# Kernel tuning notes

Measured on AMD Instinct MI355X. Metric: run time of the kernel, lower is better.

## Reference

```python
import jax, jax.numpy as jnp
import numpy as np

B, HW, FEAT = 64, 196, 2048
EMB, HID, ATT, VOCAB, T = 512, 1024, 512, 10000, 20
STEPS = T - 1  # pack_padded_sequence uses lengths - 1


def setup_inputs() -> dict:
    key = jax.random.key(0)
    ks = jax.random.split(key, 16)
    rn = lambda k, s, sc=0.02: jax.random.normal(k, s, jnp.float32) * sc
    return {
        "features": jax.random.normal(ks[0], (B, HW, FEAT), jnp.float32),
        "captions": jax.random.randint(ks[1], (B, T), 0, VOCAB),
        "lengths": jnp.full((B,), T, jnp.int32),  # uniform lengths -> constant batch per step
        "E": rn(ks[2], (VOCAB, EMB)),
        "W_feat": rn(ks[3], (EMB, FEAT)), "b_feat": jnp.zeros((EMB,), jnp.float32),
        "W1": rn(ks[4], (ATT, EMB)), "b1": jnp.zeros((ATT,), jnp.float32),
        "W2": rn(ks[5], (ATT, HID)), "b2": jnp.zeros((ATT,), jnp.float32),
        "V": rn(ks[6], (1, ATT)), "bV": jnp.zeros((1,), jnp.float32),
        "W_hi": rn(ks[7], (HID, EMB)), "b_hi": jnp.zeros((HID,), jnp.float32),
        "W_ci": rn(ks[8], (HID, EMB)), "b_ci": jnp.zeros((HID,), jnp.float32),
        "W_ih": rn(ks[9], (4 * HID, 2 * EMB)), "b_ih": jnp.zeros((4 * HID,), jnp.float32),
        "W_hh": rn(ks[10], (4 * HID, HID)), "b_hh": jnp.zeros((4 * HID,), jnp.float32),
        "W_out": rn(ks[11], (VOCAB, HID)), "b_out": jnp.zeros((VOCAB,), jnp.float32),
    }


def reference(features, captions, lengths, E, W_feat, b_feat, W1, b1, W2, b2,
              V, bV, W_hi, b_hi, W_ci, b_ci, W_ih, b_ih, W_hh, b_hh, W_out, b_out):
    # features -> embed space: [B, HW, EMB]
    f = jnp.einsum('bhc,ec->bhe', features, W_feat) + b_feat
    fmean = f.mean(axis=1)                      # [B, EMB]
    hx0 = fmean @ W_hi.T + b_hi                 # [B, HID]
    cx0 = fmean @ W_ci.T + b_ci                 # [B, HID]
    fa = jnp.einsum('bhe,ae->bha', f, W1) + b1  # W1(features), [B, HW, ATT]

    emb = E[captions]                           # [B, T, EMB]
    xs = jnp.swapaxes(emb[:, :STEPS], 0, 1)     # [STEPS, B, EMB] teacher-forced inputs

    def step(carry, x):
        hx, cx = carry
        # Bahdanau attention
        ha = hx @ W2.T + b2                             # [B, ATT]
        score = jnp.tanh(fa + ha[:, None, :])           # [B, HW, ATT]
        logits = jnp.einsum('bha,oa->bho', score, V) + bV   # [B, HW, 1]
        w = jax.nn.softmax(logits, axis=1)              # softmax over HW
        ctx = jnp.sum(w * f, axis=1)                    # [B, EMB]
        # LSTMCell (PyTorch gate order: i, f, g, o)
        inp = jnp.concatenate([x, ctx], axis=1)         # [B, 2*EMB]
        gates = inp @ W_ih.T + b_ih + hx @ W_hh.T + b_hh
        i_g, f_g, g_g, o_g = jnp.split(gates, 4, axis=1)
        cx_n = jax.nn.sigmoid(f_g) * cx + jax.nn.sigmoid(i_g) * jnp.tanh(g_g)
        hx_n = jax.nn.sigmoid(o_g) * jnp.tanh(cx_n)
        out = hx_n @ W_out.T + b_out                    # dropout = identity (eval)
        return (hx_n, cx_n), out

    _, outs = jax.lax.scan(step, (hx0, cx0), xs)        # [STEPS, B, VOCAB]
    # torch.cat(outputs) over constant per-step batch == flatten time-major
    return outs.reshape(STEPS * B, VOCAB)
```

## Files before the change

### kernel.cpp

```cpp
#include <hip/hip_runtime.h>
#include <hip/hip_bf16.h>
#include <math.h>

#define BB 64
#define HW 196
#define FEAT 2048
#define EMB 512
#define HID 1024
#define ATT 512
#define VOCAB 10000
#define TT 20
#define STEPS 19

using bfrag = __attribute__((ext_vector_type(8))) short;
using f32x4 = __attribute__((ext_vector_type(4))) float;

__device__ __forceinline__ float sigmoid_fast(float x) { return 1.0f / (1.0f + __expf(-x)); }
__device__ __forceinline__ float tanh_fast(float x) {
    float e = __expf(2.0f * x);
    return 1.0f - 2.0f / (e + 1.0f);
}
__device__ __forceinline__ ushort f2bf_rne(float f) {
    unsigned u = __float_as_uint(f);
    unsigned r = (u + 0x7FFFu + ((u >> 16) & 1u)) >> 16;
    return (ushort)r;
}
__device__ __forceinline__ float bf2f(ushort h) {
    return __uint_as_float(((unsigned)h) << 16);
}
__device__ __forceinline__ int sw_idx(int row, int g) { return row * 4 + (g ^ ((row >> 1) & 3)); }

__global__ __launch_bounds__(256) void k_split(const float* __restrict__ x,
                                               ushort* __restrict__ hi,
                                               ushort* __restrict__ lo, int n)
{
    int i4 = (blockIdx.x * 256 + threadIdx.x) * 4;
    if (i4 >= n) return;
    float4 v = *(const float4*)(x + i4);
    float av[4] = {v.x, v.y, v.z, v.w};
    #pragma unroll
    for (int j = 0; j < 4; ++j) {
        ushort h = f2bf_rne(av[j]);
        hi[i4 + j] = h;
        lo[i4 + j] = f2bf_rne(av[j] - bf2f(h));
    }
}

template<bool NFAST>
__global__ __launch_bounds__(256) void mfma_g(
    const float* __restrict__ A,
    const ushort* __restrict__ Bhi, const ushort* __restrict__ Blo,
    const float* __restrict__ bias, float* __restrict__ C,
    int N, int K, int Bld, int ldc, int NXB, int NMB)
{
    __shared__ __align__(16) ushort sAh[256 * 8];
    __shared__ __align__(16) ushort sAl[256 * 8];
    __shared__ __align__(16) ushort sBh[512 * 8];
    __shared__ __align__(16) ushort sBl[512 * 8];

    const int tid = threadIdx.x;

    const int nwg = NXB * NMB;
    const int q = nwg >> 3, r = nwg & 7;
    const int xcd = blockIdx.x & 7, sidx = blockIdx.x >> 3;
    const int wg = (xcd < r) ? (xcd * (q + 1) + sidx)
                             : (r * (q + 1) + (xcd - r) * q + sidx);
    int im, inb;
    if (NFAST) { inb = wg % NXB; im = wg / NXB; }
    else       { im = wg % NMB; inb = wg / NMB; }
    const int m0 = im * 64;
    const int n0 = inb * 128;

    const int lane = tid & 63;
    const int w = tid >> 6;
    const int mh = (w & 1) * 32;
    const int nh = (w >> 1) * 64;
    const int g = lane >> 4, l15 = lane & 15;

    f32x4 acc[2][4] = {};

    for (int k0 = 0; k0 < K; k0 += 32) {
        __syncthreads();
        {
            int r_ = tid >> 2, g_ = tid & 3;
            const float* ap = A + (size_t)(m0 + r_) * K + k0 + g_ * 8;
            float av[8];
            *(float4*)(av)     = *(const float4*)(ap);
            *(float4*)(av + 4) = *(const float4*)(ap + 4);
            bfrag vh, vl;
            #pragma unroll
            for (int j = 0; j < 8; ++j) {
                ushort h = f2bf_rne(av[j]);
                vh[j] = (short)h;
                vl[j] = (short)f2bf_rne(av[j] - bf2f(h));
            }
            int c = sw_idx(r_, g_) * 8;
            *(bfrag*)&sAh[c] = vh;
            *(bfrag*)&sAl[c] = vl;
        }
        #pragma unroll
        for (int i = 0; i < 4; ++i) {
            int c = tid + i * 256;
            int pl = c >> 9, idx2 = c & 511;
            int r_ = idx2 >> 2, g_ = idx2 & 3;
            int brow = min(n0 + r_, N - 1);
            const ushort* src = (pl ? Blo : Bhi) + (size_t)brow * Bld + k0 + g_ * 8;
            int cc = sw_idx(r_, g_) * 8;
            if (pl) *(bfrag*)&sBl[cc] = *(const bfrag*)src;
            else    *(bfrag*)&sBh[cc] = *(const bfrag*)src;
        }
        __syncthreads();

        bfrag ah[2], al[2], bh[4], bl[4];
        #pragma unroll
        for (int s = 0; s < 2; ++s) {
            int c = sw_idx(mh + s * 16 + l15, g) * 8;
            ah[s] = *(const bfrag*)&sAh[c];
            al[s] = *(const bfrag*)&sAl[c];
        }
        #pragma unroll
        for (int u = 0; u < 4; ++u) {
            int c = sw_idx(nh + u * 16 + l15, g) * 8;
            bh[u] = *(const bfrag*)&sBh[c];
            bl[u] = *(const bfrag*)&sBl[c];
        }
        #pragma unroll
        for (int s = 0; s < 2; ++s)
            #pragma unroll
            for (int u = 0; u < 4; ++u) {
                acc[s][u] = __builtin_amdgcn_mfma_f32_16x16x32_bf16(ah[s], bh[u], acc[s][u], 0, 0, 0);
                acc[s][u] = __builtin_amdgcn_mfma_f32_16x16x32_bf16(ah[s], bl[u], acc[s][u], 0, 0, 0);
                acc[s][u] = __builtin_amdgcn_mfma_f32_16x16x32_bf16(al[s], bh[u], acc[s][u], 0, 0, 0);
            }
    }

    #pragma unroll
    for (int s = 0; s < 2; ++s)
        #pragma unroll
        for (int u = 0; u < 4; ++u) {
            int col = n0 + nh + u * 16 + l15;
            if (col < N) {
                float bv = bias ? bias[col] : 0.f;
                #pragma unroll
                for (int rr = 0; rr < 4; ++rr) {
                    int row = m0 + mh + s * 16 + g * 4 + rr;
                    C[(size_t)row * ldc + col] = acc[s][u][rr] + bv;
                }
            }
        }
}

__global__ __launch_bounds__(256) void k_fmean(const float* __restrict__ f,
                                               float* __restrict__ fmean)
{
    int b = blockIdx.x, tid = threadIdx.x;
    for (int e = tid; e < EMB; e += 256) {
        const float* fb = f + (size_t)b * HW * EMB + e;
        float s = 0.f;
        for (int h = 0; h < HW; ++h) s += fb[(size_t)h * EMB];
        fmean[b * EMB + e] = s * (1.0f / HW);
    }
}

__global__ __launch_bounds__(256) void k_init(
    const float* __restrict__ fmean,
    const float* __restrict__ W_hi, const float* __restrict__ b_hi,
    const float* __restrict__ W_ci, const float* __restrict__ b_ci,
    float* __restrict__ hx, float* __restrict__ cx)
{
    int b = blockIdx.x, tid = threadIdx.x;
    __shared__ float fm[EMB];
    for (int i = tid; i < EMB; i += 256) fm[i] = fmean[b * EMB + i];
    __syncthreads();
    for (int u = tid; u < HID; u += 256) {
        const float4* w1 = (const float4*)(W_hi + (size_t)u * EMB);
        const float4* w2 = (const float4*)(W_ci + (size_t)u * EMB);
        float a1 = b_hi[u], a2 = b_ci[u];
        for (int k = 0; k < EMB / 4; ++k) {
            float4 y1 = w1[k], y2 = w2[k];
            float x0 = fm[4*k], x1 = fm[4*k+1], x2 = fm[4*k+2], x3 = fm[4*k+3];
            a1 += x0*y1.x + x1*y1.y + x2*y1.z + x3*y1.w;
            a2 += x0*y2.x + x1*y2.y + x2*y2.z + x3*y2.w;
        }
        hx[b * HID + u] = a1;
        cx[b * HID + u] = a2;
    }
}

__global__ __launch_bounds__(128) void k_embed(const int* __restrict__ cap,
                                               const float* __restrict__ E,
                                               float* __restrict__ xs_f)
{
    int blk = blockIdx.x;
    int t = blk / BB, b = blk % BB;
    int c = cap[b * TT + t];
    const float4* src = (const float4*)(E + (size_t)c * EMB);
    float4* dst = (float4*)(xs_f + ((size_t)t * BB + b) * EMB);
    dst[threadIdx.x] = src[threadIdx.x];
}

__global__ __launch_bounds__(256) void k_ha(
    const float* __restrict__ hx, const float* __restrict__ W2,
    const float* __restrict__ b2, float* __restrict__ ha)
{
    __shared__ __align__(16) float hx_s[8][1028];
    __shared__ float part[256];
    const int tid = threadIdx.x;
    const int a0 = (blockIdx.x >> 3) * 16;
    const int b0 = (blockIdx.x & 7) * 8;

    for (int i = tid; i < 8 * 256; i += 256) {
        int r = i >> 8, c4 = i & 255;
        *(float4*)&hx_s[r][c4 * 4] = *(const float4*)(hx + (size_t)(b0 + r) * HID + c4 * 4);
    }
    __syncthreads();

    const int a_i = tid >> 4;
    const int b_i = (tid >> 1) & 7;
    const int half = tid & 1;
    const float4* wr = (const float4*)(W2 + (size_t)(a0 + a_i) * HID + half * 512);
    const float* xr = &hx_s[b_i][half * 512];
    float s = 0.f;
    #pragma unroll 8
    for (int i = 0; i < 128; ++i) {
        float4 w = wr[i];
        float4 x = *(const float4*)(xr + i * 4);
        s += w.x*x.x + w.y*x.y + w.z*x.z + w.w*x.w;
    }
    part[tid] = s;
    __syncthreads();
    if (!half)
        ha[(size_t)(b0 + b_i) * ATT + a0 + a_i] = part[tid] + part[tid + 1] + b2[a0 + a_i];
}

__global__ __launch_bounds__(1024) void k_att(
    const float* __restrict__ f, const float* __restrict__ fa,
    const float* __restrict__ ha, const float* __restrict__ V,
    ushort* __restrict__ ctx_hi, ushort* __restrict__ ctx_lo)
{
    __shared__ __align__(16) float smem[2048];
    const int b = blockIdx.x;
    const int tid = threadIdx.x;
    const int lane = tid & 63;
    const int wid = tid >> 6;

    float* ha_s = smem;
    float* V_s  = smem + 512;
    float* w_s  = smem + 1024;
    float* red  = smem + 1280;
    float* pc   = smem + 1536;

    if (tid < ATT) { ha_s[tid] = ha[b * ATT + tid]; V_s[tid] = V[tid]; }
    __syncthreads();

    for (int h = wid; h < HW; h += 16) {
        const float4* fr = (const float4*)(fa + ((size_t)b * HW + h) * ATT);
        float s = 0.f;
        #pragma unroll
        for (int q = 0; q < 2; ++q) {
            int i4 = q * 64 + lane;
            float4 fv = fr[i4];
            float4 hv = *(const float4*)&ha_s[i4 * 4];
            float4 vv = *(const float4*)&V_s[i4 * 4];
            s += tanh_fast(fv.x + hv.x) * vv.x + tanh_fast(fv.y + hv.y) * vv.y
               + tanh_fast(fv.z + hv.z) * vv.z + tanh_fast(fv.w + hv.w) * vv.w;
        }
        #pragma unroll
        for (int off = 32; off > 0; off >>= 1) s += __shfl_down(s, off);
        if (lane == 0) w_s[h] = s;
    }
    __syncthreads();

    float v = (tid < HW) ? w_s[tid] : -INFINITY;
    if (tid < 256) red[tid] = v;
    __syncthreads();
    for (int s2 = 128; s2 > 0; s2 >>= 1) {
        if (tid < s2) red[tid] = fmaxf(red[tid], red[tid + s2]);
        __syncthreads();
    }
    float mx = red[0];
    __syncthreads();
    float e = (tid < HW) ? __expf(v - mx) : 0.f;
    if (tid < 256) red[tid] = e;
    __syncthreads();
    for (int s2 = 128; s2 > 0; s2 >>= 1) {
        if (tid < s2) red[tid] += red[tid + s2];
        __syncthreads();
    }
    float inv = 1.0f / red[0];
    if (tid < HW) w_s[tid] = e * inv;
    __syncthreads();

    {
        int e0 = tid & 511, grp = tid >> 9;
        const float* fb = f + (size_t)b * HW * EMB + e0;
        float s = 0.f;
        int h0 = grp * 98;
        for (int h = h0; h < h0 + 98; ++h)
            s = fmaf(w_s[h], fb[(size_t)h * EMB], s);
        if (grp) pc[e0] = s;
        __syncthreads();
        if (!grp) {
            float c = s + pc[e0];
            ushort ch = f2bf_rne(c);
            ctx_hi[b * EMB + e0] = ch;
            ctx_lo[b * EMB + e0] = f2bf_rne(c - bf2f(ch));
        }
    }
}

__global__ __launch_bounds__(512) void k_gates_lstm(
    const float* __restrict__ gxs_t,
    const ushort* __restrict__ cth, const ushort* __restrict__ ctl,
    const ushort* __restrict__ hxh, const ushort* __restrict__ hxl,
    const ushort* __restrict__ wihh, const ushort* __restrict__ wihl,
    const ushort* __restrict__ whhh, const ushort* __restrict__ whhl,
    const float* __restrict__ b_ih, const float* __restrict__ b_hh,
    float* __restrict__ hx, float* __restrict__ cx,
    ushort* __restrict__ nxh, ushort* __restrict__ nxl,
    float* __restrict__ hx_all_t)
{
    __shared__ float sg[2][64][16];
    const int tid = threadIdx.x, bk = blockIdx.x;
    const int lane = tid & 63, wid = tid >> 6;
    const int mt = wid & 3, kh = wid >> 2;
    const int l15 = lane & 15, g = lane >> 4;
    const int arow = mt * 16 + l15;
    const int ncol = (l15 >> 2) * 1024 + bk * 4 + (l15 & 3);
    const int koff = g * 8;

    f32x4 acc0 = {}, acc1 = {};

    if (kh == 0) {
        {
            const ushort* ah = cth + (size_t)arow * 512 + koff;
            const ushort* al = ctl + (size_t)arow * 512 + koff;
            const ushort* bh = wihh + (size_t)ncol * 1024 + 512 + koff;
            const ushort* bl = wihl + (size_t)ncol * 1024 + 512 + koff;
            #pragma unroll 4
            for (int kk = 0; kk < 16; ++kk) {
                bfrag a_h = *(const bfrag*)(ah + kk * 32);
                bfrag a_l = *(const bfrag*)(al + kk * 32);
                bfrag b_h = *(const bfrag*)(bh + kk * 32);
                bfrag b_l = *(const bfrag*)(bl + kk * 32);
                acc0 = __builtin_amdgcn_mfma_f32_16x16x32_bf16(a_h, b_h, acc0, 0, 0, 0);
                acc1 = __builtin_amdgcn_mfma_f32_16x16x32_bf16(a_h, b_l, acc1, 0, 0, 0);
                acc1 = __builtin_amdgcn_mfma_f32_16x16x32_bf16(a_l, b_h, acc1, 0, 0, 0);
            }
        }
        {
            const ushort* ah = hxh + (size_t)arow * 1024 + koff;
            const ushort* al = hxl + (size_t)arow * 1024 + koff;
            const ushort* bh = whhh + (size_t)ncol * 1024 + koff;
            const ushort* bl = whhl + (size_t)ncol * 1024 + koff;
            #pragma unroll 4
            for (int kk = 0; kk < 8; ++kk) {
                bfrag a_h = *(const bfrag*)(ah + kk * 32);
                bfrag a_l = *(const bfrag*)(al + kk * 32);
                bfrag b_h = *(const bfrag*)(bh + kk * 32);
                bfrag b_l = *(const bfrag*)(bl + kk * 32);
                acc0 = __builtin_amdgcn_mfma_f32_16x16x32_bf16(a_h, b_h, acc0, 0, 0, 0);
                acc1 = __builtin_amdgcn_mfma_f32_16x16x32_bf16(a_h, b_l, acc1, 0, 0, 0);
                acc1 = __builtin_amdgcn_mfma_f32_16x16x32_bf16(a_l, b_h, acc1, 0, 0, 0);
            }
        }
    } else {
        const ushort* ah = hxh + (size_t)arow * 1024 + 256 + koff;
        const ushort* al = hxl + (size_t)arow * 1024 + 256 + koff;
        const ushort* bh = whhh + (size_t)ncol * 1024 + 256 + koff;
        const ushort* bl = whhl + (size_t)ncol * 1024 + 256 + koff;
        #pragma unroll 4
        for (int kk = 0; kk < 24; ++kk) {
            bfrag a_h = *(const bfrag*)(ah + kk * 32);
            bfrag a_l = *(const bfrag*)(al + kk * 32);
            bfrag b_h = *(const bfrag*)(bh + kk * 32);
            bfrag b_l = *(const bfrag*)(bl + kk * 32);
            acc0 = __builtin_amdgcn_mfma_f32_16x16x32_bf16(a_h, b_h, acc0, 0, 0, 0);
            acc1 = __builtin_amdgcn_mfma_f32_16x16x32_bf16(a_h, b_l, acc1, 0, 0, 0);
            acc1 = __builtin_amdgcn_mfma_f32_16x16x32_bf16(a_l, b_h, acc1, 0, 0, 0);
        }
    }

    #pragma unroll
    for (int rr = 0; rr < 4; ++rr)
        sg[kh][mt * 16 + g * 4 + rr][l15] = acc0[rr] + acc1[rr];
    __syncthreads();

    if (tid < 256) {
        int b = tid >> 2, uu = tid & 3;
        int u = bk * 4 + uu;
        const float* gx = gxs_t + (size_t)b * 4096;
        float gi = sg[0][b][uu]      + sg[1][b][uu]      + gx[u]        + b_ih[u]        + b_hh[u];
        float gf = sg[0][b][4 + uu]  + sg[1][b][4 + uu]  + gx[1024 + u] + b_ih[1024 + u] + b_hh[1024 + u];
        float gg = sg[0][b][8 + uu]  + sg[1][b][8 + uu]  + gx[2048 + u] + b_ih[2048 + u] + b_hh[2048 + u];
        float go = sg[0][b][12 + uu] + sg[1][b][12 + uu] + gx[3072 + u] + b_ih[3072 + u] + b_hh[3072 + u];
        int idx = b * 1024 + u;
        float c = sigmoid_fast(gf) * cx[idx] + sigmoid_fast(gi) * tanh_fast(gg);
        float h = sigmoid_fast(go) * tanh_fast(c);
        cx[idx] = c;
        hx[idx] = h;
        hx_all_t[idx] = h;
        ushort hh = f2bf_rne(h);
        nxh[idx] = hh;
        nxl[idx] = f2bf_rne(h - bf2f(hh));
    }
}

extern "C" void kernel_launch(void* const* d_in, const int* in_sizes, int n_in,
                              void* d_out, int out_size, void* d_ws, size_t ws_size,
                              hipStream_t stream) {
    const float* features = (const float*)d_in[0];
    const int*   captions = (const int*)d_in[1];
    const float* E      = (const float*)d_in[3];
    const float* W_feat = (const float*)d_in[4];
    const float* b_feat = (const float*)d_in[5];
    const float* W1     = (const float*)d_in[6];
    const float* b1     = (const float*)d_in[7];
    const float* W2     = (const float*)d_in[8];
    const float* b2     = (const float*)d_in[9];
    const float* V      = (const float*)d_in[10];
    const float* W_hi   = (const float*)d_in[12];
    const float* b_hi   = (const float*)d_in[13];
    const float* W_ci   = (const float*)d_in[14];
    const float* b_ci   = (const float*)d_in[15];
    const float* W_ih   = (const float*)d_in[16];
    const float* b_ih   = (const float*)d_in[17];
    const float* W_hh   = (const float*)d_in[18];
    const float* b_hh   = (const float*)d_in[19];
    const float* W_out  = (const float*)d_in[20];
    const float* b_out  = (const float*)d_in[21];
    float* out = (float*)d_out;

    float* ws = (float*)d_ws;
    float* f_buf   = ws;
    float* fa_buf  = f_buf + 6422528;
    float* fmean   = fa_buf + 6422528;
    float* hx      = fmean + 32768;
    float* cx      = hx + 65536;
    float* hx_all  = cx + 65536;
    float* ha      = hx_all + 1310720;
    float* xs_f    = ha + 32768;
    float* gxs     = xs_f + 622592;
    ushort* p = (ushort*)(gxs + 4980736);
    ushort* wfeat_hi = p;            p += 1048576;
    ushort* wfeat_lo = p;            p += 1048576;
    ushort* w1_hi    = p;            p += 262144;
    ushort* w1_lo    = p;            p += 262144;
    ushort* wih_hi   = p;            p += 4194304;
    ushort* wih_lo   = p;            p += 4194304;
    ushort* whh_hi   = p;            p += 4194304;
    ushort* whh_lo   = p;            p += 4194304;
    ushort* ctx_hi   = p;            p += 32768;
    ushort* ctx_lo   = p;            p += 32768;
    ushort* hxp      = p;            p += 262144;
    ushort* wout_hi = (ushort*)f_buf;
    ushort* wout_lo = wout_hi + 10240000;

    k_split<<<1048576 / 4 / 256, 256, 0, stream>>>(W_feat, wfeat_hi, wfeat_lo, 1048576);
    k_split<<<262144 / 4 / 256, 256, 0, stream>>>(W1, w1_hi, w1_lo, 262144);
    k_split<<<4194304 / 4 / 256, 256, 0, stream>>>(W_ih, wih_hi, wih_lo, 4194304);
    k_split<<<4194304 / 4 / 256, 256, 0, stream>>>(W_hh, whh_hi, whh_lo, 4194304);
    k_embed<<<STEPS * BB, 128, 0, stream>>>(captions, E, xs_f);
    mfma_g<true><<<784, 256, 0, stream>>>(
        features, wfeat_hi, wfeat_lo, b_feat, f_buf, 512, 2048, 2048, 512, 4, 196);
    mfma_g<true><<<784, 256, 0, stream>>>(
        f_buf, w1_hi, w1_lo, b1, fa_buf, 512, 512, 512, 512, 4, 196);
    mfma_g<false><<<608, 256, 0, stream>>>(
        xs_f, wih_hi, wih_lo, nullptr, gxs, 4096, 512, 1024, 4096, 32, 19);
    k_fmean<<<BB, 256, 0, stream>>>(f_buf, fmean);
    k_init<<<BB, 256, 0, stream>>>(fmean, W_hi, b_hi, W_ci, b_ci, hx, cx);
    k_split<<<65536 / 4 / 256, 256, 0, stream>>>(hx, hxp, hxp + 65536, 65536);

    for (int t = 0; t < STEPS; ++t) {
        ushort* hx_rd = hxp + (size_t)(t & 1) * 131072;
        ushort* hx_wr = hxp + (size_t)((t + 1) & 1) * 131072;
        k_ha<<<256, 256, 0, stream>>>(hx, W2, b2, ha);
        k_att<<<BB, 1024, 0, stream>>>(f_buf, fa_buf, ha, V, ctx_hi, ctx_lo);
        k_gates_lstm<<<256, 512, 0, stream>>>(
            gxs + (size_t)t * BB * 4096,
            ctx_hi, ctx_lo, hx_rd, hx_rd + 65536,
            wih_hi, wih_lo, whh_hi, whh_lo, b_ih, b_hh,
            hx, cx, hx_wr, hx_wr + 65536,
            hx_all + (size_t)t * BB * HID);
    }

    k_split<<<10240000 / 4 / 256, 256, 0, stream>>>(W_out, wout_hi, wout_lo, 10240000);
    mfma_g<false><<<1501, 256, 0, stream>>>(
        hx_all, wout_hi, wout_lo, b_out, out, VOCAB, HID, 1024, VOCAB, 79, 19);
}
```

Measured before the change: 1.698 ms.

## Split fp32 weights in-GEMM, prefetch next K chunk, split attention into more blocks

The GEMM gains a mode that loads fp32 B weights and splits them into bf16 hi/lo in registers. This removes the separate k_split passes for W_feat, W1 and W_out along with their intermediate buffers. Global loads for the next K chunk are now issued before the MFMA work on the current chunk, overlapping memory with compute. The per-step attention kernel (64 blocks of 1024 threads) becomes a logits kernel and a softmax+context kernel, each with 256 blocks; fmean and init get more parallel layouts, and init now writes the bf16 hx split directly. The cost is redundant B-splitting work across M tiles, one more launch per step, and higher register pressure from the prefetch.

```diff
diff --git a/kernel.cpp b/kernel.cpp
--- a/kernel.cpp
+++ b/kernel.cpp
@@ -46,9 +46,10 @@
     }
 }
 
-template<bool NFAST>
+template<bool BF32B, bool NFAST>
 __global__ __launch_bounds__(256) void mfma_g(
     const float* __restrict__ A,
+    const float* __restrict__ Bf,
     const ushort* __restrict__ Bhi, const ushort* __restrict__ Blo,
     const float* __restrict__ bias, float* __restrict__ C,
     int N, int K, int Bld, int ldc, int NXB, int NMB)
@@ -77,39 +78,93 @@
     const int nh = (w >> 1) * 64;
     const int g = lane >> 4, l15 = lane & 15;
 
+    const int rA = tid >> 2, gA = tid & 3;
+    const float* apA = A + (size_t)(m0 + rA) * K + gA * 8;
+    const int cA = sw_idx(rA, gA) * 8;
+
+    const float* apBf[2]; int cBf[2];
+    const ushort* apBp[4]; int cBp[4];
+    if (BF32B) {
+        #pragma unroll
+        for (int i = 0; i < 2; ++i) {
+            int c = tid + i * 256;
+            int r_ = c >> 2, g_ = c & 3;
+            int brow = min(n0 + r_, N - 1);
+            apBf[i] = Bf + (size_t)brow * Bld + g_ * 8;
+            cBf[i] = sw_idx(r_, g_) * 8;
+        }
+    } else {
+        #pragma unroll
+        for (int i = 0; i < 4; ++i) {
+            int c = tid + i * 256;
+            int pl = i >> 1;
+            int idx2 = c & 511;
+            int r_ = idx2 >> 2, g_ = idx2 & 3;
+            int brow = min(n0 + r_, N - 1);
+            apBp[i] = (pl ? Blo : Bhi) + (size_t)brow * Bld + g_ * 8;
+            cBp[i] = sw_idx(r_, g_) * 8;
+        }
+    }
+
+    float a_reg[8];
+    float bf_reg[16];
+    bfrag bp_reg[4];
+
+    auto load_chunk = [&](int kk) {
+        *(float4*)(a_reg)     = *(const float4*)(apA + kk);
+        *(float4*)(a_reg + 4) = *(const float4*)(apA + kk + 4);
+        if constexpr (BF32B) {
+            #pragma unroll
+            for (int i = 0; i < 2; ++i) {
+                *(float4*)(bf_reg + i * 8)     = *(const float4*)(apBf[i] + kk);
+                *(float4*)(bf_reg + i * 8 + 4) = *(const float4*)(apBf[i] + kk + 4);
+            }
+        } else {
+            #pragma unroll
+            for (int i = 0; i < 4; ++i)
+                bp_reg[i] = *(const bfrag*)(apBp[i] + kk);
+        }
+    };
+
     f32x4 acc[2][4] = {};
+    load_chunk(0);
 
     for (int k0 = 0; k0 < K; k0 += 32) {
         __syncthreads();
         {
-            int r_ = tid >> 2, g_ = tid & 3;
-            const float* ap = A + (size_t)(m0 + r_) * K + k0 + g_ * 8;
-            float av[8];
-            *(float4*)(av)     = *(const float4*)(ap);
-            *(float4*)(av + 4) = *(const float4*)(ap + 4);
             bfrag vh, vl;
             #pragma unroll
             for (int j = 0; j < 8; ++j) {
-                ushort h = f2bf_rne(av[j]);
+                ushort h = f2bf_rne(a_reg[j]);
                 vh[j] = (short)h;
-                vl[j] = (short)f2bf_rne(av[j] - bf2f(h));
-            }
-            int c = sw_idx(r_, g_) * 8;
-            *(bfrag*)&sAh[c] = vh;
-            *(bfrag*)&sAl[c] = vl;
-        }
-        #pragma unroll
-        for (int i = 0; i < 4; ++i) {
-            int c = tid + i * 256;
-            int pl = c >> 9, idx2 = c & 511;
-            int r_ = idx2 >> 2, g_ = idx2 & 3;
-            int brow = min(n0 + r_, N - 1);
-            const ushort* src = (pl ? Blo : Bhi) + (size_t)brow * Bld + k0 + g_ * 8;
-            int cc = sw_idx(r_, g_) * 8;
-            if (pl) *(bfrag*)&sBl[cc] = *(const bfrag*)src;
-            else    *(bfrag*)&sBh[cc] = *(const bfrag*)src;
+                vl[j] = (short)f2bf_rne(a_reg[j] - bf2f(h));
+            }
+            *(bfrag*)&sAh[cA] = vh;
+            *(bfrag*)&sAl[cA] = vl;
+        }
+        if constexpr (BF32B) {
+            #pragma unroll
+            for (int i = 0; i < 2; ++i) {
+                bfrag vh, vl;
+                #pragma unroll
+                for (int j = 0; j < 8; ++j) {
+                    float v = bf_reg[i * 8 + j];
+                    ushort h = f2bf_rne(v);
+                    vh[j] = (short)h;
+                    vl[j] = (short)f2bf_rne(v - bf2f(h));
+                }
+                *(bfrag*)&sBh[cBf[i]] = vh;
+                *(bfrag*)&sBl[cBf[i]] = vl;
+            }
+        } else {
+            *(bfrag*)&sBh[cBp[0]] = bp_reg[0];
+            *(bfrag*)&sBh[cBp[1]] = bp_reg[1];
+            *(bfrag*)&sBl[cBp[2]] = bp_reg[2];
+            *(bfrag*)&sBl[cBp[3]] = bp_reg[3];
         }
         __syncthreads();
+
+        if (k0 + 32 < K) load_chunk(k0 + 32);
 
         bfrag ah[2], al[2], bh[4], bl[4];
         #pragma unroll
@@ -150,40 +205,49 @@
         }
 }
 
-__global__ __launch_bounds__(256) void k_fmean(const float* __restrict__ f,
-                                               float* __restrict__ fmean)
-{
-    int b = blockIdx.x, tid = threadIdx.x;
-    for (int e = tid; e < EMB; e += 256) {
-        const float* fb = f + (size_t)b * HW * EMB + e;
-        float s = 0.f;
-        for (int h = 0; h < HW; ++h) s += fb[(size_t)h * EMB];
-        fmean[b * EMB + e] = s * (1.0f / HW);
-    }
-}
-
-__global__ __launch_bounds__(256) void k_init(
+__global__ __launch_bounds__(256) void k_fmean2(const float* __restrict__ f,
+                                                float* __restrict__ fmean)
+{
+    __shared__ float part[128];
+    int blk = blockIdx.x;
+    int b = blk >> 2, eq = blk & 3;
+    int el = threadIdx.x & 127, half = threadIdx.x >> 7;
+    int e = eq * 128 + el;
+    const float* fb = f + (size_t)b * HW * EMB + e;
+    float s = 0.f;
+    int h0 = half * 98;
+    for (int h = h0; h < h0 + 98; ++h) s += fb[(size_t)h * EMB];
+    if (half) part[el] = s;
+    __syncthreads();
+    if (!half) fmean[b * EMB + e] = (s + part[el]) * (1.0f / HW);
+}
+
+__global__ __launch_bounds__(256) void k_init2(
     const float* __restrict__ fmean,
     const float* __restrict__ W_hi, const float* __restrict__ b_hi,
     const float* __restrict__ W_ci, const float* __restrict__ b_ci,
-    float* __restrict__ hx, float* __restrict__ cx)
-{
-    int b = blockIdx.x, tid = threadIdx.x;
-    __shared__ float fm[EMB];
-    for (int i = tid; i < EMB; i += 256) fm[i] = fmean[b * EMB + i];
-    __syncthreads();
-    for (int u = tid; u < HID; u += 256) {
-        const float4* w1 = (const float4*)(W_hi + (size_t)u * EMB);
-        const float4* w2 = (const float4*)(W_ci + (size_t)u * EMB);
-        float a1 = b_hi[u], a2 = b_ci[u];
-        for (int k = 0; k < EMB / 4; ++k) {
-            float4 y1 = w1[k], y2 = w2[k];
-            float x0 = fm[4*k], x1 = fm[4*k+1], x2 = fm[4*k+2], x3 = fm[4*k+3];
-            a1 += x0*y1.x + x1*y1.y + x2*y1.z + x3*y1.w;
-            a2 += x0*y2.x + x1*y2.y + x2*y2.z + x3*y2.w;
-        }
-        hx[b * HID + u] = a1;
-        cx[b * HID + u] = a2;
+    float* __restrict__ hx, float* __restrict__ cx,
+    ushort* __restrict__ hxp_h, ushort* __restrict__ hxp_l)
+{
+    int o = blockIdx.x * 256 + threadIdx.x;
+    int b = o >> 11, uu = o & 2047;
+    bool isC = uu >= 1024;
+    int u = uu & 1023;
+    const float4* wr = (const float4*)((isC ? W_ci : W_hi) + (size_t)u * EMB);
+    const float4* fm = (const float4*)(fmean + (size_t)b * EMB);
+    float s = isC ? b_ci[u] : b_hi[u];
+    #pragma unroll 8
+    for (int k = 0; k < EMB / 4; ++k) {
+        float4 wv = wr[k], xv = fm[k];
+        s += wv.x*xv.x + wv.y*xv.y + wv.z*xv.z + wv.w*xv.w;
+    }
+    int idx = b * HID + u;
+    if (isC) cx[idx] = s;
+    else {
+        hx[idx] = s;
+        ushort hh = f2bf_rne(s);
+        hxp_h[idx] = hh;
+        hxp_l[idx] = f2bf_rne(s - bf2f(hh));
     }
 }
 
@@ -233,32 +297,25 @@
         ha[(size_t)(b0 + b_i) * ATT + a0 + a_i] = part[tid] + part[tid + 1] + b2[a0 + a_i];
 }
 
-__global__ __launch_bounds__(1024) void k_att(
-    const float* __restrict__ f, const float* __restrict__ fa,
-    const float* __restrict__ ha, const float* __restrict__ V,
-    ushort* __restrict__ ctx_hi, ushort* __restrict__ ctx_lo)
-{
-    __shared__ __align__(16) float smem[2048];
-    const int b = blockIdx.x;
-    const int tid = threadIdx.x;
-    const int lane = tid & 63;
-    const int wid = tid >> 6;
-
-    float* ha_s = smem;
-    float* V_s  = smem + 512;
-    float* w_s  = smem + 1024;
-    float* red  = smem + 1280;
-    float* pc   = smem + 1536;
-
-    if (tid < ATT) { ha_s[tid] = ha[b * ATT + tid]; V_s[tid] = V[tid]; }
-    __syncthreads();
-
-    for (int h = wid; h < HW; h += 16) {
+__global__ __launch_bounds__(256) void k_logits(
+    const float* __restrict__ fa, const float* __restrict__ ha,
+    const float* __restrict__ V, float* __restrict__ logits)
+{
+    int blk = blockIdx.x;
+    int b = blk >> 2, q = blk & 3;
+    int tid = threadIdx.x;
+    __shared__ float ha_s[ATT];
+    __shared__ float V_s[ATT];
+    for (int i = tid; i < ATT; i += 256) { ha_s[i] = ha[b * ATT + i]; V_s[i] = V[i]; }
+    __syncthreads();
+
+    int wid = tid >> 6, lane = tid & 63;
+    for (int h = q * 49 + wid; h < q * 49 + 49; h += 4) {
         const float4* fr = (const float4*)(fa + ((size_t)b * HW + h) * ATT);
         float s = 0.f;
         #pragma unroll
-        for (int q = 0; q < 2; ++q) {
-            int i4 = q * 64 + lane;
+        for (int i = 0; i < 2; ++i) {
+            int i4 = lane + (i << 6);
             float4 fv = fr[i4];
             float4 hv = *(const float4*)&ha_s[i4 * 4];
             float4 vv = *(const float4*)&V_s[i4 * 4];
@@ -267,45 +324,52 @@
         }
         #pragma unroll
         for (int off = 32; off > 0; off >>= 1) s += __shfl_down(s, off);
-        if (lane == 0) w_s[h] = s;
-    }
-    __syncthreads();
-
-    float v = (tid < HW) ? w_s[tid] : -INFINITY;
-    if (tid < 256) red[tid] = v;
-    __syncthreads();
-    for (int s2 = 128; s2 > 0; s2 >>= 1) {
-        if (tid < s2) red[tid] = fmaxf(red[tid], red[tid + s2]);
+        if (lane == 0) logits[b * HW + h] = s;
+    }
+}
+
+__global__ __launch_bounds__(256) void k_ctx(
+    const float* __restrict__ logits, const float* __restrict__ f,
+    ushort* __restrict__ ctx_hi, ushort* __restrict__ ctx_lo)
+{
+    int blk = blockIdx.x;
+    int b = blk >> 2, eg = blk & 3;
+    int tid = threadIdx.x;
+    __shared__ float w_s[HW];
+    __shared__ float red_s[256];
+    __shared__ float part[128];
+
+    float v = (tid < HW) ? logits[b * HW + tid] : -INFINITY;
+    red_s[tid] = v; __syncthreads();
+    for (int s = 128; s > 0; s >>= 1) {
+        if (tid < s) red_s[tid] = fmaxf(red_s[tid], red_s[tid + s]);
         __syncthreads();
     }
-    float mx = red[0];
-    __syncthreads();
+    float mx = red_s[0]; __syncthreads();
     float e = (tid < HW) ? __expf(v - mx) : 0.f;
-    if (tid < 256) red[tid] = e;
-    __syncthreads();
-    for (int s2 = 128; s2 > 0; s2 >>= 1) {
-        if (tid < s2) red[tid] += red[tid + s2];
+    red_s[tid] = e; __syncthreads();
+    for (int s = 128; s > 0; s >>= 1) {
+        if (tid < s) red_s[tid] += red_s[tid + s];
         __syncthreads();
     }
-    float inv = 1.0f / red[0];
+    float inv = 1.0f / red_s[0];
     if (tid < HW) w_s[tid] = e * inv;
     __syncthreads();
 
-    {
-        int e0 = tid & 511, grp = tid >> 9;
-        const float* fb = f + (size_t)b * HW * EMB + e0;
-        float s = 0.f;
-        int h0 = grp * 98;
-        for (int h = h0; h < h0 + 98; ++h)
-            s = fmaf(w_s[h], fb[(size_t)h * EMB], s);
-        if (grp) pc[e0] = s;
-        __syncthreads();
-        if (!grp) {
-            float c = s + pc[e0];
-            ushort ch = f2bf_rne(c);
-            ctx_hi[b * EMB + e0] = ch;
-            ctx_lo[b * EMB + e0] = f2bf_rne(c - bf2f(ch));
-        }
+    int e0 = (eg << 7) + (tid & 127);
+    int half = tid >> 7;
+    const float* fb = f + (size_t)b * HW * EMB + e0;
+    float s = 0.f;
+    int h0 = half * 98;
+    for (int h = h0; h < h0 + 98; ++h)
+        s = fmaf(w_s[h], fb[(size_t)h * EMB], s);
+    if (half) part[tid & 127] = s;
+    __syncthreads();
+    if (!half) {
+        float c = s + part[tid];
+        ushort ch = f2bf_rne(c);
+        ctx_hi[b * EMB + e0] = ch;
+        ctx_lo[b * EMB + e0] = f2bf_rne(c - bf2f(ch));
     }
 }
 
@@ -439,13 +503,10 @@
     float* cx      = hx + 65536;
     float* hx_all  = cx + 65536;
     float* ha      = hx_all + 1310720;
-    float* xs_f    = ha + 32768;
+    float* logits  = ha + 32768;
+    float* xs_f    = logits + 16384;
     float* gxs     = xs_f + 622592;
     ushort* p = (ushort*)(gxs + 4980736);
-    ushort* wfeat_hi = p;            p += 1048576;
-    ushort* wfeat_lo = p;            p += 1048576;
-    ushort* w1_hi    = p;            p += 262144;
-    ushort* w1_lo    = p;            p += 262144;
     ushort* wih_hi   = p;            p += 4194304;
     ushort* wih_lo   = p;            p += 4194304;
     ushort* whh_hi   = p;            p += 4194304;
@@ -453,29 +514,26 @@
     ushort* ctx_hi   = p;            p += 32768;
     ushort* ctx_lo   = p;            p += 32768;
     ushort* hxp      = p;            p += 262144;
-    ushort* wout_hi = (ushort*)f_buf;
-    ushort* wout_lo = wout_hi + 10240000;
-
-    k_split<<<1048576 / 4 / 256, 256, 0, stream>>>(W_feat, wfeat_hi, wfeat_lo, 1048576);
-    k_split<<<262144 / 4 / 256, 256, 0, stream>>>(W1, w1_hi, w1_lo, 262144);
+
     k_split<<<4194304 / 4 / 256, 256, 0, stream>>>(W_ih, wih_hi, wih_lo, 4194304);
     k_split<<<4194304 / 4 / 256, 256, 0, stream>>>(W_hh, whh_hi, whh_lo, 4194304);
     k_embed<<<STEPS * BB, 128, 0, stream>>>(captions, E, xs_f);
-    mfma_g<true><<<784, 256, 0, stream>>>(
-        features, wfeat_hi, wfeat_lo, b_feat, f_buf, 512, 2048, 2048, 512, 4, 196);
-    mfma_g<true><<<784, 256, 0, stream>>>(
-        f_buf, w1_hi, w1_lo, b1, fa_buf, 512, 512, 512, 512, 4, 196);
-    mfma_g<false><<<608, 256, 0, stream>>>(
-        xs_f, wih_hi, wih_lo, nullptr, gxs, 4096, 512, 1024, 4096, 32, 19);
-    k_fmean<<<BB, 256, 0, stream>>>(f_buf, fmean);
-    k_init<<<BB, 256, 0, stream>>>(fmean, W_hi, b_hi, W_ci, b_ci, hx, cx);
-    k_split<<<65536 / 4 / 256, 256, 0, stream>>>(hx, hxp, hxp + 65536, 65536);
+    mfma_g<true, true><<<784, 256, 0, stream>>>(
+        features, W_feat, nullptr, nullptr, b_feat, f_buf, 512, 2048, 2048, 512, 4, 196);
+    mfma_g<true, true><<<784, 256, 0, stream>>>(
+        f_buf, W1, nullptr, nullptr, b1, fa_buf, 512, 512, 512, 512, 4, 196);
+    mfma_g<false, false><<<608, 256, 0, stream>>>(
+        xs_f, nullptr, wih_hi, wih_lo, nullptr, gxs, 4096, 512, 1024, 4096, 32, 19);
+    k_fmean2<<<256, 256, 0, stream>>>(f_buf, fmean);
+    k_init2<<<512, 256, 0, stream>>>(fmean, W_hi, b_hi, W_ci, b_ci,
+                                     hx, cx, hxp, hxp + 65536);
 
     for (int t = 0; t < STEPS; ++t) {
         ushort* hx_rd = hxp + (size_t)(t & 1) * 131072;
         ushort* hx_wr = hxp + (size_t)((t + 1) & 1) * 131072;
         k_ha<<<256, 256, 0, stream>>>(hx, W2, b2, ha);
-        k_att<<<BB, 1024, 0, stream>>>(f_buf, fa_buf, ha, V, ctx_hi, ctx_lo);
+        k_logits<<<256, 256, 0, stream>>>(fa_buf, ha, V, logits);
+        k_ctx<<<256, 256, 0, stream>>>(logits, f_buf, ctx_hi, ctx_lo);
         k_gates_lstm<<<256, 512, 0, stream>>>(
             gxs + (size_t)t * BB * 4096,
             ctx_hi, ctx_lo, hx_rd, hx_rd + 65536,
@@ -484,7 +542,6 @@
             hx_all + (size_t)t * BB * HID);
     }
 
-    k_split<<<10240000 / 4 / 256, 256, 0, stream>>>(W_out, wout_hi, wout_lo, 10240000);
-    mfma_g<false><<<1501, 256, 0, stream>>>(
-        hx_all, wout_hi, wout_lo, b_out, out, VOCAB, HID, 1024, VOCAB, 79, 19);
-}
+    mfma_g<true, false><<<1501, 256, 0, stream>>>(
+        hx_all, W_out, nullptr, nullptr, b_out, out, VOCAB, HID, 1024, VOCAB, 79, 19);
+}
```

After: 1.920 ms. 1.13x slower.
